# Kernel tuning notes

Measured on AMD Instinct MI355X. Metric: run time of the kernel, lower is better.

The kernel has to match this reference:

```python
import jax, jax.numpy as jnp
import numpy as np

N_COLS = 107
CAT_SLICES = [(1, 10), (10, 26), (27, 34), (34, 49), (49, 55), (55, 60), (60, 62), (65, 107)]
MSE_COLS = [0, 26, 62, 63, 64]
BATCH = 524288


def setup_inputs() -> dict:
    key = jax.random.key(0)
    k_dec, k_cont, k_cat = jax.random.split(key, 3)
    data_decoded = jax.random.normal(k_dec, (BATCH, N_COLS), dtype=jnp.float32)
    # Build data_true: continuous cols random, categorical slices exactly one-hot.
    data_true = jax.random.uniform(k_cont, (BATCH, N_COLS), dtype=jnp.float32)
    rows = jnp.arange(BATCH)
    for i, (s, e) in enumerate(CAT_SLICES):
        kk = jax.random.fold_in(k_cat, i)
        labels = jax.random.randint(kk, (BATCH,), 0, e - s)
        data_true = data_true.at[:, s:e].set(0.0)
        data_true = data_true.at[rows, s + labels].set(1.0)
    return {"data_decoded": data_decoded, "data_true": data_true, "batch_size": BATCH}


def _ce(logits, onehot_true):
    # torch nonzero()[:,1] on an exact one-hot slice == argmax
    labels = jnp.argmax(onehot_true, axis=1)
    logp = jax.nn.log_softmax(logits, axis=1)
    return -jnp.mean(jnp.take_along_axis(logp, labels[:, None], axis=1))


def _mse(a, b):
    d = a - b
    return jnp.mean(d * d)


def reference(data_decoded, data_true, batch_size):
    mse_loss = jnp.float32(0.0)
    for c in MSE_COLS:
        mse_loss = mse_loss + _mse(data_decoded[:, c], data_true[:, c])
    ce_loss = jnp.float32(0.0)
    for s, e in CAT_SLICES:
        ce_loss = ce_loss + _ce(data_decoded[:, s:e], data_true[:, s:e])
    multi_loss = mse_loss + ce_loss
    return multi_loss, mse_loss, ce_loss
```

## Files before the change

### kernel.cpp

```cpp
#include <hip/hip_runtime.h>

#define NCOLS 107
#define TROWS 64
#define TELEMS (TROWS * NCOLS)
#define TVEC  (TELEMS / 4)

template<int S, int E>
__device__ __forceinline__ float slice_ce_lds(const float* dr, const float* tr) {
    constexpr int L = E - S;
    float v[L];
#pragma unroll
    for (int j = 0; j < L; ++j) v[j] = dr[S + j];
    float m = v[0];
#pragma unroll
    for (int j = 1; j < L; ++j) m = fmaxf(m, v[j]);
    float sum = 0.0f, dot = 0.0f;
#pragma unroll
    for (int j = 0; j < L; ++j) {
        sum += __expf(v[j] - m);
        dot = fmaf(v[j], tr[S + j], dot);
    }
    return m + __logf(sum) - dot;
}

__global__ __launch_bounds__(256, 2) void multiloss_main(
        const float* __restrict__ dec, const float* __restrict__ tru,
        float2* __restrict__ ws, int nrows) {
    __shared__ float4 sdec4[TVEC];
    __shared__ float4 stru4[TVEC];
    const float* sdec = (const float*)sdec4;
    const float* stru = (const float*)stru4;

    int tile0 = blockIdx.x * TROWS;
    int rows_here = nrows - tile0;
    if (rows_here > TROWS) rows_here = TROWS;
    size_t base = (size_t)tile0 * NCOLS;

    if (rows_here == TROWS) {
        const float4* gd = (const float4*)(dec + base);
        const float4* gt = (const float4*)(tru + base);
        for (int i = threadIdx.x; i < TVEC; i += 256) {
            sdec4[i] = gd[i];
            stru4[i] = gt[i];
        }
    } else {
        int n = rows_here * NCOLS;
        float* sd = (float*)sdec4;
        float* st = (float*)stru4;
        for (int i = threadIdx.x; i < n; i += 256) {
            sd[i] = dec[base + i];
            st[i] = tru[base + i];
        }
    }
    __syncthreads();

    int row  = threadIdx.x >> 2;
    int part = threadIdx.x & 3;
    float mse = 0.0f, ce = 0.0f;
    if (row < rows_here) {
        const float* dr = sdec + row * NCOLS;
        const float* tr = stru + row * NCOLS;
        if (part == 0) {
            ce += slice_ce_lds<65, 107>(dr, tr);
        } else if (part == 1) {
            ce += slice_ce_lds<10, 26>(dr, tr);
            ce += slice_ce_lds<34, 49>(dr, tr);
        } else if (part == 2) {
            ce += slice_ce_lds<1, 10>(dr, tr);
            ce += slice_ce_lds<27, 34>(dr, tr);
            ce += slice_ce_lds<49, 55>(dr, tr);
        } else {
            ce += slice_ce_lds<55, 60>(dr, tr);
            ce += slice_ce_lds<60, 62>(dr, tr);
            float d;
            d = dr[0]  - tr[0];  mse = fmaf(d, d, mse);
            d = dr[26] - tr[26]; mse = fmaf(d, d, mse);
            d = dr[62] - tr[62]; mse = fmaf(d, d, mse);
            d = dr[63] - tr[63]; mse = fmaf(d, d, mse);
            d = dr[64] - tr[64]; mse = fmaf(d, d, mse);
        }
    }

#pragma unroll
    for (int off = 32; off > 0; off >>= 1) {
        mse += __shfl_down(mse, off, 64);
        ce  += __shfl_down(ce,  off, 64);
    }
    __shared__ float smse[4], sce[4];
    int wid  = threadIdx.x >> 6;
    int lane = threadIdx.x & 63;
    if (lane == 0) { smse[wid] = mse; sce[wid] = ce; }
    __syncthreads();
    if (threadIdx.x == 0) {
        float bm = smse[0] + smse[1] + smse[2] + smse[3];
        float bc = sce[0]  + sce[1]  + sce[2]  + sce[3];
        ws[blockIdx.x] = make_float2(bm, bc);
    }
}

__global__ __launch_bounds__(256) void multiloss_fin(
        const float2* __restrict__ ws, float* __restrict__ out,
        int nblocks, float invN) {
    float m = 0.0f, c = 0.0f;
    for (int i = threadIdx.x; i < nblocks; i += 256) {
        float2 v = ws[i];
        m += v.x; c += v.y;
    }
#pragma unroll
    for (int off = 32; off > 0; off >>= 1) {
        m += __shfl_down(m, off, 64);
        c += __shfl_down(c, off, 64);
    }
    __shared__ float sm[4], sc[4];
    int wid  = threadIdx.x >> 6;
    int lane = threadIdx.x & 63;
    if (lane == 0) { sm[wid] = m; sc[wid] = c; }
    __syncthreads();
    if (threadIdx.x == 0) {
        float mse = (sm[0] + sm[1] + sm[2] + sm[3]) * invN;
        float ce  = (sc[0] + sc[1] + sc[2] + sc[3]) * invN;
        out[0] = mse + ce;
        out[1] = mse;
        out[2] = ce;
    }
}

extern "C" void kernel_launch(void* const* d_in, const int* in_sizes, int n_in,
                              void* d_out, int out_size, void* d_ws, size_t ws_size,
                              hipStream_t stream) {
    const float* dec = (const float*)d_in[0];
    const float* tru = (const float*)d_in[1];
    int nrows = in_sizes[0] / NCOLS;
    int nblocks = (nrows + TROWS - 1) / TROWS;
    float2* ws = (float2*)d_ws;
    multiloss_main<<<nblocks, 256, 0, stream>>>(dec, tru, ws, nrows);
    multiloss_fin<<<1, 256, 0, stream>>>(ws, (float*)d_out, nblocks,
                                         1.0f / (float)nrows);
}
```

Before: 460.2 us.

## Fuse target dot and MSE into load pass, drop target LDS tile, persistent grid

The CE target term is now computed during the global load as a dot product of decoded and true values over all non-MSE columns, relying on the one-hot targets, so the true tile no longer needs to be staged in shared memory. The LDS footprint is halved, tiles shrink to 32 rows with 128-thread blocks, and a fixed grid of 4096 blocks loops over tiles. The aim is higher occupancy, less LDS traffic, and fewer partial sums for the final reduction. The per-element column modulo and select logic adds ALU work during the load, and only half the threads take part in the per-row LSE phase.

```diff
diff --git a/kernel.cpp b/kernel.cpp
--- a/kernel.cpp
+++ b/kernel.cpp
@@ -1,12 +1,14 @@
 #include <hip/hip_runtime.h>
 
 #define NCOLS 107
-#define TROWS 64
-#define TELEMS (TROWS * NCOLS)
-#define TVEC  (TELEMS / 4)
+#define TROWS 32
+#define TFLOATS (TROWS * NCOLS)
+#define TVEC (TFLOATS / 4)
+#define THREADS 128
+#define GRID 4096
 
 template<int S, int E>
-__device__ __forceinline__ float slice_ce_lds(const float* dr, const float* tr) {
+__device__ __forceinline__ float slice_lse(const float* dr) {
     constexpr int L = E - S;
     float v[L];
 #pragma unroll
@@ -14,88 +16,97 @@
     float m = v[0];
 #pragma unroll
     for (int j = 1; j < L; ++j) m = fmaxf(m, v[j]);
-    float sum = 0.0f, dot = 0.0f;
+    float s = 0.0f;
 #pragma unroll
-    for (int j = 0; j < L; ++j) {
-        sum += __expf(v[j] - m);
-        dot = fmaf(v[j], tr[S + j], dot);
-    }
-    return m + __logf(sum) - dot;
+    for (int j = 0; j < L; ++j) s += __expf(v[j] - m);
+    return m + __logf(s);
 }
 
-__global__ __launch_bounds__(256, 2) void multiloss_main(
+__device__ __forceinline__ bool is_mse_col(int c) {
+    return (c == 0) | (c == 26) | ((unsigned)(c - 62) <= 2u);
+}
+
+__global__ __launch_bounds__(THREADS) void multiloss_main(
         const float* __restrict__ dec, const float* __restrict__ tru,
-        float2* __restrict__ ws, int nrows) {
+        float2* __restrict__ ws, int nrows, int ntiles) {
     __shared__ float4 sdec4[TVEC];
-    __shared__ float4 stru4[TVEC];
-    const float* sdec = (const float*)sdec4;
-    const float* stru = (const float*)stru4;
+    float* sdec = (float*)sdec4;
 
-    int tile0 = blockIdx.x * TROWS;
-    int rows_here = nrows - tile0;
-    if (rows_here > TROWS) rows_here = TROWS;
-    size_t base = (size_t)tile0 * NCOLS;
+    float mse = 0.0f, dot = 0.0f, lse = 0.0f;
 
-    if (rows_here == TROWS) {
-        const float4* gd = (const float4*)(dec + base);
-        const float4* gt = (const float4*)(tru + base);
-        for (int i = threadIdx.x; i < TVEC; i += 256) {
-            sdec4[i] = gd[i];
-            stru4[i] = gt[i];
+    for (int tile = blockIdx.x; tile < ntiles; tile += GRID) {
+        size_t base = (size_t)tile * TFLOATS;
+        int rows_here = nrows - tile * TROWS;
+        if (rows_here > TROWS) rows_here = TROWS;
+
+        __syncthreads();
+
+        if (rows_here == TROWS) {
+            const float4* gd = (const float4*)(dec + base);
+            const float4* gt = (const float4*)(tru + base);
+#pragma unroll
+            for (int it = 0; it < 7; ++it) {
+                int fi = it * THREADS + threadIdx.x;
+                if (fi < TVEC) {
+                    float4 dv = gd[fi];
+                    float4 tv = gt[fi];
+                    sdec4[fi] = dv;
+                    int c0 = (fi * 4) % NCOLS;
+                    float dk[4] = {dv.x, dv.y, dv.z, dv.w};
+                    float tk[4] = {tv.x, tv.y, tv.z, tv.w};
+#pragma unroll
+                    for (int k = 0; k < 4; ++k) {
+                        int c = c0 + k; if (c >= NCOLS) c -= NCOLS;
+                        float d = dk[k], t = tk[k];
+                        float df = d - t;
+                        mse += is_mse_col(c) ? df * df : 0.0f;
+                        dot += is_mse_col(c) ? 0.0f : d * t;
+                    }
+                }
+            }
+        } else {
+            int n = rows_here * NCOLS;
+            for (int i = threadIdx.x; i < n; i += THREADS) {
+                float d = dec[base + i], t = tru[base + i];
+                sdec[i] = d;
+                int c = i % NCOLS;
+                float df = d - t;
+                mse += is_mse_col(c) ? df * df : 0.0f;
+                dot += is_mse_col(c) ? 0.0f : d * t;
+            }
         }
-    } else {
-        int n = rows_here * NCOLS;
-        float* sd = (float*)sdec4;
-        float* st = (float*)stru4;
-        for (int i = threadIdx.x; i < n; i += 256) {
-            sd[i] = dec[base + i];
-            st[i] = tru[base + i];
-        }
-    }
-    __syncthreads();
+        __syncthreads();
 
-    int row  = threadIdx.x >> 2;
-    int part = threadIdx.x & 3;
-    float mse = 0.0f, ce = 0.0f;
-    if (row < rows_here) {
-        const float* dr = sdec + row * NCOLS;
-        const float* tr = stru + row * NCOLS;
-        if (part == 0) {
-            ce += slice_ce_lds<65, 107>(dr, tr);
-        } else if (part == 1) {
-            ce += slice_ce_lds<10, 26>(dr, tr);
-            ce += slice_ce_lds<34, 49>(dr, tr);
-        } else if (part == 2) {
-            ce += slice_ce_lds<1, 10>(dr, tr);
-            ce += slice_ce_lds<27, 34>(dr, tr);
-            ce += slice_ce_lds<49, 55>(dr, tr);
-        } else {
-            ce += slice_ce_lds<55, 60>(dr, tr);
-            ce += slice_ce_lds<60, 62>(dr, tr);
-            float d;
-            d = dr[0]  - tr[0];  mse = fmaf(d, d, mse);
-            d = dr[26] - tr[26]; mse = fmaf(d, d, mse);
-            d = dr[62] - tr[62]; mse = fmaf(d, d, mse);
-            d = dr[63] - tr[63]; mse = fmaf(d, d, mse);
-            d = dr[64] - tr[64]; mse = fmaf(d, d, mse);
+        int row  = threadIdx.x >> 2;
+        int part = threadIdx.x & 3;
+        if (row < rows_here) {
+            const float* dr = sdec + row * NCOLS;
+            if (part == 0) {
+                lse += slice_lse<65, 107>(dr);
+            } else if (part == 1) {
+                lse += slice_lse<10, 26>(dr) + slice_lse<34, 49>(dr);
+            } else if (part == 2) {
+                lse += slice_lse<1, 10>(dr) + slice_lse<27, 34>(dr)
+                     + slice_lse<49, 55>(dr);
+            } else {
+                lse += slice_lse<55, 60>(dr) + slice_lse<60, 62>(dr);
+            }
         }
     }
 
+    float ce = lse - dot;
 #pragma unroll
     for (int off = 32; off > 0; off >>= 1) {
         mse += __shfl_down(mse, off, 64);
         ce  += __shfl_down(ce,  off, 64);
     }
-    __shared__ float smse[4], sce[4];
+    __shared__ float sm[2], sc[2];
     int wid  = threadIdx.x >> 6;
     int lane = threadIdx.x & 63;
-    if (lane == 0) { smse[wid] = mse; sce[wid] = ce; }
+    if (lane == 0) { sm[wid] = mse; sc[wid] = ce; }
     __syncthreads();
-    if (threadIdx.x == 0) {
-        float bm = smse[0] + smse[1] + smse[2] + smse[3];
-        float bc = sce[0]  + sce[1]  + sce[2]  + sce[3];
-        ws[blockIdx.x] = make_float2(bm, bc);
-    }
+    if (threadIdx.x == 0)
+        ws[blockIdx.x] = make_float2(sm[0] + sm[1], sc[0] + sc[1]);
 }
 
 __global__ __launch_bounds__(256) void multiloss_fin(
@@ -130,10 +141,10 @@
                               hipStream_t stream) {
     const float* dec = (const float*)d_in[0];
     const float* tru = (const float*)d_in[1];
-    int nrows = in_sizes[0] / NCOLS;
-    int nblocks = (nrows + TROWS - 1) / TROWS;
+    int nrows  = in_sizes[0] / NCOLS;
+    int ntiles = (nrows + TROWS - 1) / TROWS;
     float2* ws = (float2*)d_ws;
-    multiloss_main<<<nblocks, 256, 0, stream>>>(dec, tru, ws, nrows);
-    multiloss_fin<<<1, 256, 0, stream>>>(ws, (float*)d_out, nblocks,
+    multiloss_main<<<GRID, THREADS, 0, stream>>>(dec, tru, ws, nrows, ntiles);
+    multiloss_fin<<<1, 256, 0, stream>>>(ws, (float*)d_out, GRID,
                                          1.0f / (float)nrows);
 }
```

After: 449.3 us. 1.02x faster.
